# Kernel optimization log

Hardware: AMD Instinct MI355X
Metric: run time of the kernel (lower is better)

## Reference

```python
import jax, jax.numpy as jnp
import numpy as np

B, S, D = 8, 2048, 768

def setup_inputs() -> dict:
    key = jax.random.key(0)
    k1, k2, k3, k4 = jax.random.split(key, 4)
    scale = 1.0 / np.sqrt(D)
    x = jax.random.normal(k1, (B, S, D), dtype=jnp.float32)
    W = jax.random.normal(k2, (D, D), dtype=jnp.float32) * scale
    proj_w = jax.random.normal(k3, (D, D), dtype=jnp.float32) * scale
    proj_b = jax.random.normal(k4, (D,), dtype=jnp.float32) * scale
    return {"x": x, "W": W, "proj_w": proj_w, "proj_b": proj_b}


def reference(x, W, proj_w, proj_b):
    # Wx = Linear(x) with torch convention: x @ W.T  -> [B,S,D]
    Wx = jnp.einsum('bsd,ed->bse', x, W)
    # s = Wx @ x^T  -> [B,S,S]
    s = jnp.einsum('bse,bte->bst', Wx, x)
    # mask diagonal (self) with -inf
    eye = jnp.eye(S, dtype=bool)
    s = jnp.where(eye[None, :, :], -jnp.inf, s)
    a = jax.nn.softmax(s, axis=2)
    # c = a @ x -> [B,S,D]
    c = jnp.einsum('bst,btd->bsd', a, x)
    # proj + relu, residual; dropout with p=0 is identity
    c = jax.nn.relu(jnp.einsum('bsd,ed->bse', c, proj_w) + proj_b)
    return x + c
```

## Files before the change

### kernel.cpp

```cpp
#include <hip/hip_runtime.h>
#include <hip/hip_bf16.h>

typedef _Float16 fp16_t;
typedef __attribute__((ext_vector_type(8))) _Float16 fp16x8;
typedef __attribute__((ext_vector_type(4))) _Float16 fp16x4;
typedef __attribute__((ext_vector_type(4))) float fx4;

#define GLDS(g, l)                                                              \
  __builtin_amdgcn_global_load_lds(                                             \
      (const __attribute__((address_space(1))) void*)(g),                       \
      (__attribute__((address_space(3))) void*)(l), 16, 0, 0)

#define PBAR()                                                                  \
  do {                                                                          \
    __builtin_amdgcn_sched_barrier(0);                                          \
    __builtin_amdgcn_s_barrier();                                               \
    __builtin_amdgcn_sched_barrier(0);                                          \
  } while (0)

enum { EPI_F32 = 0, EPI_F16 = 1, EPI_FUSE = 2, EPI_SOFT = 3 };

__device__ __forceinline__ void xcd_decode(int& bx, int& by, int& bz) {
  const int nx = gridDim.x, ny = gridDim.y;
  const int lid = (int)(blockIdx.x + nx * (blockIdx.y + ny * blockIdx.z));
  const int j = lid & 7, k = lid >> 3;
  bx = k % nx;
  const int s = j + 8 * (k / nx);
  by = s % ny;
  bz = s / ny;
}

template <bool ASPLIT, int EPI>
__global__ __launch_bounds__(256) void gemm_bt(
    const fp16_t* __restrict__ A1, const fp16_t* __restrict__ A2,
    const fp16_t* __restrict__ B1, void* __restrict__ Cv, int K, int lda,
    int ldb, long long sA, long long sB, long long sC,
    const float* __restrict__ bias, const float* __restrict__ resid,
    float* __restrict__ m_out, float* __restrict__ l_out) {
  constexpr int ALO = ASPLIT ? 128 * 32 : 0;
  __shared__ __align__(16) fp16_t As[2][128 * 32 + ALO];
  __shared__ __align__(16) fp16_t Bs[2][128 * 32];
  __shared__ float smax[(EPI == EPI_SOFT) ? 256 : 1];
  __shared__ float ssum[(EPI == EPI_SOFT) ? 256 : 1];

  const int tid  = threadIdx.x;
  const int lane = tid & 63;
  const int w    = tid >> 6;
  const int wr   = w >> 1;
  const int wc   = w & 1;

  int bx, by, bz;
  xcd_decode(bx, by, bz);
  const int N = (int)gridDim.x * 128;
  const long long tile_m = (long long)by * 128;
  const long long tile_n = (long long)bx * 128;
  const long long z = bz;
  const long long aoff = z * sA + tile_m * (long long)lda;
  const long long boff = z * sB + tile_n * (long long)ldb;

  fx4 acc[4][4];
#pragma unroll
  for (int i = 0; i < 4; i++)
#pragma unroll
    for (int j = 0; j < 4; j++) acc[i][j] = (fx4){0.f, 0.f, 0.f, 0.f};

  const int r_l = lane >> 2;
  const int c_l = ((((lane & 3) + ((r_l >> 1) & 3)) & 3) << 3);
  const int frow = lane & 15;
  const int qoff = (((lane >> 4) - ((frow >> 1) & 3)) & 3) << 3;

  const size_t sa0 = (size_t)(w * 16 + r_l) * lda + c_l;
  const size_t sa1 = (size_t)(64 + w * 16 + r_l) * lda + c_l;
  const size_t sb0 = (size_t)(w * 16 + r_l) * ldb + c_l;
  const size_t sb1 = (size_t)(64 + w * 16 + r_l) * ldb + c_l;
  const int ld0 = (w * 16) * 32;
  const int ld1 = (64 + w * 16) * 32;

  auto stage = [&](int b, int kk) {
    const fp16_t* gah = A1 + aoff + kk;
    const fp16_t* gbh = B1 + boff + kk;
    GLDS(gah + sa0, &As[b][ld0]);
    GLDS(gah + sa1, &As[b][ld1]);
    GLDS(gbh + sb0, &Bs[b][ld0]);
    GLDS(gbh + sb1, &Bs[b][ld1]);
    if (ASPLIT) {
      const fp16_t* gal = A2 + aoff + kk;
      GLDS(gal + sa0, &As[b][ALO + ld0]);
      GLDS(gal + sa1, &As[b][ALO + ld1]);
    }
  };
  auto compute = [&](int b) {
    fp16x8 afh[4], bbh[4], afl[4];
#pragma unroll
    for (int mi = 0; mi < 4; mi++)
      afh[mi] = *(const fp16x8*)&As[b][(wr * 64 + mi * 16 + frow) * 32 + qoff];
#pragma unroll
    for (int ni = 0; ni < 4; ni++)
      bbh[ni] = *(const fp16x8*)&Bs[b][(wc * 64 + ni * 16 + frow) * 32 + qoff];
    if (ASPLIT) {
#pragma unroll
      for (int mi = 0; mi < 4; mi++)
        afl[mi] =
            *(const fp16x8*)&As[b][ALO + (wr * 64 + mi * 16 + frow) * 32 + qoff];
    }
#pragma unroll
    for (int mi = 0; mi < 4; mi++)
#pragma unroll
      for (int ni = 0; ni < 4; ni++) {
        fx4 a = acc[mi][ni];
        a = __builtin_amdgcn_mfma_f32_16x16x32_f16(afh[mi], bbh[ni], a, 0, 0, 0);
        if (ASPLIT)
          a = __builtin_amdgcn_mfma_f32_16x16x32_f16(afl[mi], bbh[ni], a, 0, 0, 0);
        acc[mi][ni] = a;
      }
  };

  stage(0, 0);
  for (int kt = 0; kt < K; kt += 64) {
    stage(1, kt + 32);
    if (ASPLIT) asm volatile("s_waitcnt vmcnt(6)" ::: "memory");
    else        asm volatile("s_waitcnt vmcnt(4)" ::: "memory");
    PBAR();
    compute(0);
    PBAR();
    if (kt + 64 < K) {
      stage(0, kt + 64);
      if (ASPLIT) asm volatile("s_waitcnt vmcnt(6)" ::: "memory");
      else        asm volatile("s_waitcnt vmcnt(4)" ::: "memory");
    } else {
      asm volatile("s_waitcnt vmcnt(0)" ::: "memory");
    }
    PBAR();
    compute(1);
    PBAR();
  }

  const int er = (lane >> 4) * 4;
  const int ec = lane & 15;
  const long long crow = tile_m + wr * 64;
  const long long ccol = tile_n + wc * 64;

  if constexpr (EPI == EPI_SOFT) {
#pragma unroll
    for (int mi = 0; mi < 4; mi++)
#pragma unroll
      for (int j = 0; j < 4; j++) {
        const long long r = crow + mi * 16 + er + j;
        float mx = -1e30f;
#pragma unroll
        for (int ni = 0; ni < 4; ni++) {
          const long long cc = ccol + ni * 16 + ec;
          float v = acc[mi][ni][j];
          if (r == cc) v = -1e30f;
          acc[mi][ni][j] = v;
          mx = fmaxf(mx, v);
        }
#pragma unroll
        for (int o = 1; o < 16; o <<= 1) mx = fmaxf(mx, __shfl_xor(mx, o, 64));
        if (ec == 0) smax[wc * 128 + wr * 64 + mi * 16 + er + j] = mx;
      }
    __syncthreads();
#pragma unroll
    for (int mi = 0; mi < 4; mi++)
#pragma unroll
      for (int j = 0; j < 4; j++) {
        const int rid = wr * 64 + mi * 16 + er + j;
        const float m = fmaxf(smax[rid], smax[128 + rid]);
        const long long r = crow + mi * 16 + er + j;
        float s = 0.f;
#pragma unroll
        for (int ni = 0; ni < 4; ni++) {
          const float e = __expf(acc[mi][ni][j] - m);
          s += e;
          ((fp16_t*)Cv)[z * sC + r * N + (ccol + ni * 16 + ec)] = (fp16_t)e;
        }
#pragma unroll
        for (int o = 1; o < 16; o <<= 1) s += __shfl_xor(s, o, 64);
        if (ec == 0) ssum[wc * 128 + rid] = s;
      }
    __syncthreads();
    if (tid < 128) {
      const long long si = (z * 16 + bx) * 2048 + tile_m + tid;
      m_out[si] = fmaxf(smax[tid], smax[128 + tid]);
      l_out[si] = ssum[tid] + ssum[128 + tid];
    }
  } else {
#pragma unroll
    for (int mi = 0; mi < 4; mi++)
#pragma unroll
      for (int j = 0; j < 4; j++) {
        const long long r = crow + mi * 16 + er + j;
#pragma unroll
        for (int ni = 0; ni < 4; ni++) {
          const long long cc = ccol + ni * 16 + ec;
          const long long idx = z * sC + r * N + cc;
          const float v = acc[mi][ni][j];
          if (EPI == EPI_F32) {
            ((float*)Cv)[idx] = v;
          } else if (EPI == EPI_F16) {
            ((fp16_t*)Cv)[idx] = (fp16_t)v;
          } else {
            float u = v + bias[cc];
            u = u > 0.f ? u : 0.f;
            ((float*)Cv)[idx] = resid[r * N + cc] + u;
          }
        }
      }
  }
}

__global__ __launch_bounds__(256) void gemm_pv(
    const fp16_t* __restrict__ P, const float* __restrict__ mstat,
    const float* __restrict__ lstat, const fp16_t* __restrict__ Bx,
    fp16_t* __restrict__ C) {
  __shared__ __align__(16) fp16_t As[2][128 * 32];
  __shared__ __align__(16) fp16_t Bs[2][128 * 32];
  __shared__ float sc[16][128];

  const int tid  = threadIdx.x;
  const int lane = tid & 63;
  const int w    = tid >> 6;
  const int wr   = w >> 1;
  const int wc   = w & 1;

  int bx, by, bz;
  xcd_decode(bx, by, bz);
  const long long tile_m = (long long)by * 128;
  const long long tile_n = (long long)bx * 128;
  const long long z = bz;

  if (tid < 128) {
    const long long base = z * 16 * 2048 + tile_m + tid;
    float mv[16];
    float m = -1e30f;
#pragma unroll
    for (int t = 0; t < 16; t++) {
      mv[t] = mstat[base + t * 2048];
      m = fmaxf(m, mv[t]);
    }
    float l = 0.f;
#pragma unroll
    for (int t = 0; t < 16; t++) l += lstat[base + t * 2048] * __expf(mv[t] - m);
    const float il = 1.0f / l;
#pragma unroll
    for (int t = 0; t < 16; t++) sc[t][tid] = __expf(mv[t] - m) * il;
  }
  __syncthreads();

  fx4 acc[4][4];
#pragma unroll
  for (int i = 0; i < 4; i++)
#pragma unroll
    for (int j = 0; j < 4; j++) acc[i][j] = (fx4){0.f, 0.f, 0.f, 0.f};

  const int r_l = lane >> 2;
  const int c_l = ((((lane & 3) + ((r_l >> 1) & 3)) & 3) << 3);
  const int frow = lane & 15;
  const int qoff = (((lane >> 4) - ((frow >> 1) & 3)) & 3) << 3;
  const size_t s0 = (size_t)(w * 16 + r_l) * 2048 + c_l;
  const size_t s1 = (size_t)(64 + w * 16 + r_l) * 2048 + c_l;
  const int ld0 = (w * 16) * 32;
  const int ld1 = (64 + w * 16) * 32;

  const fp16_t* A = P + z * (2048LL * 2048) + tile_m * 2048;
  const fp16_t* B = Bx + z * (768LL * 2048) + tile_n * 2048;

  auto stage = [&](int b, int kk) {
    GLDS(A + kk + s0, &As[b][ld0]);
    GLDS(A + kk + s1, &As[b][ld1]);
    GLDS(B + kk + s0, &Bs[b][ld0]);
    GLDS(B + kk + s1, &Bs[b][ld1]);
  };
  auto compute = [&](int b, const fp16_t* sh) {
    fp16x8 af[4], bb[4];
#pragma unroll
    for (int mi = 0; mi < 4; mi++) {
      af[mi] = *(const fp16x8*)&As[b][(wr * 64 + mi * 16 + frow) * 32 + qoff];
      af[mi] *= sh[mi];
    }
#pragma unroll
    for (int ni = 0; ni < 4; ni++)
      bb[ni] = *(const fp16x8*)&Bs[b][(wc * 64 + ni * 16 + frow) * 32 + qoff];
#pragma unroll
    for (int mi = 0; mi < 4; mi++)
#pragma unroll
      for (int ni = 0; ni < 4; ni++)
        acc[mi][ni] = __builtin_amdgcn_mfma_f32_16x16x32_f16(
            af[mi], bb[ni], acc[mi][ni], 0, 0, 0);
  };

  stage(0, 0);
  for (int kt = 0; kt < 2048; kt += 64) {
    fp16_t sh[4];
    {
      const int tt = kt >> 7;
#pragma unroll
      for (int mi = 0; mi < 4; mi++)
        sh[mi] = (fp16_t)sc[tt][wr * 64 + mi * 16 + frow];
    }
    stage(1, kt + 32);
    asm volatile("s_waitcnt vmcnt(4)" ::: "memory");
    PBAR();
    compute(0, sh);
    PBAR();
    if (kt + 64 < 2048) {
      stage(0, kt + 64);
      asm volatile("s_waitcnt vmcnt(4)" ::: "memory");
    } else {
      asm volatile("s_waitcnt vmcnt(0)" ::: "memory");
    }
    PBAR();
    compute(1, sh);
    PBAR();
  }

  const int er = (lane >> 4) * 4;
  const int ec = lane & 15;
  const long long crow = tile_m + wr * 64;
  const long long ccol = tile_n + wc * 64;
  fp16_t* Cz = C + z * (2048LL * 768);
#pragma unroll
  for (int mi = 0; mi < 4; mi++)
#pragma unroll
    for (int j = 0; j < 4; j++) {
      const long long rr = crow + mi * 16 + er + j;
#pragma unroll
      for (int ni = 0; ni < 4; ni++)
        Cz[rr * 768 + ccol + ni * 16 + ec] = (fp16_t)acc[mi][ni][j];
    }
}

__global__ __launch_bounds__(256) void prep_x(
    const float* __restrict__ x, fp16_t* __restrict__ xh,
    fp16_t* __restrict__ xl, fp16_t* __restrict__ xT) {
  __shared__ fp16_t t[32][33];
  const int b = blockIdx.z;
  const int d0 = blockIdx.x * 32;
  const int s0 = blockIdx.y * 32;
  const float* ib = x + (long long)b * 2048 * 768;
  const int tx = threadIdx.x & 31;
  const int ty = threadIdx.x >> 5;
#pragma unroll
  for (int i = 0; i < 4; i++) {
    const int srow = s0 + ty + i * 8;
    const long long idx = (long long)b * 2048 * 768 + (long long)srow * 768 + d0 + tx;
    const float v = ib[(long long)srow * 768 + d0 + tx];
    const fp16_t h = (fp16_t)v;
    xh[idx] = h;
    xl[idx] = (fp16_t)(v - (float)h);
    t[ty + i * 8][tx] = h;
  }
  __syncthreads();
#pragma unroll
  for (int i = 0; i < 4; i++)
    xT[(long long)b * 768 * 2048 + (long long)(d0 + ty + i * 8) * 2048 + s0 + tx] =
        t[tx][ty + i * 8];
}

__global__ __launch_bounds__(256) void cast2_f32_f16(
    const float* __restrict__ a, const float* __restrict__ b,
    fp16_t* __restrict__ oa, fp16_t* __restrict__ ob, int n4) {
  const int i = blockIdx.x * 256 + threadIdx.x;
  if (i >= n4) return;
  const float* in = blockIdx.y == 0 ? a : b;
  fp16_t* out = blockIdx.y == 0 ? oa : ob;
  const float4 v = ((const float4*)in)[i];
  ((fp16x4*)out)[i] =
      (fp16x4){(fp16_t)v.x, (fp16_t)v.y, (fp16_t)v.z, (fp16_t)v.w};
}

extern "C" void kernel_launch(void* const* d_in, const int* in_sizes, int n_in,
                              void* d_out, int out_size, void* d_ws,
                              size_t ws_size, hipStream_t stream) {
  const float* x  = (const float*)d_in[0];
  const float* W  = (const float*)d_in[1];
  const float* pw = (const float*)d_in[2];
  const float* pb = (const float*)d_in[3];

  const long long S = 2048, D = 768;
  const long long BS = 8 * S;

  char* p = (char*)d_ws;
  auto carve = [&](long long bytes) {
    char* q = p;
    p += (bytes + 255) & ~255LL;
    return q;
  };
  fp16_t* xh = (fp16_t*)carve(BS * D * 2);
  fp16_t* xl = (fp16_t*)carve(BS * D * 2);
  fp16_t* xT = (fp16_t*)carve(BS * D * 2);
  fp16_t* Wx = (fp16_t*)carve(BS * D * 2);
  fp16_t* Wh = (fp16_t*)carve(D * D * 2);
  fp16_t* ph = (fp16_t*)carve(D * D * 2);
  float*  mstat = (float*)carve(BS * 16 * 4);
  float*  lstat = (float*)carve(BS * 16 * 4);
  fp16_t* Ps = (fp16_t*)carve(8 * S * S * 2);
  fp16_t* cb = Wx;

  prep_x<<<dim3(24, 64, 8), 256, 0, stream>>>(x, xh, xl, xT);
  cast2_f32_f16<<<dim3((unsigned)(D * D / 4 / 256), 2), 256, 0, stream>>>(
      W, pw, Wh, ph, (int)(D * D / 4));

  gemm_bt<true, EPI_F16><<<dim3(6, 128, 1), 256, 0, stream>>>(
      xh, xl, Wh, Wx, 768, 768, 768, 0, 0, 0, nullptr, nullptr, nullptr,
      nullptr);

  gemm_bt<false, EPI_SOFT><<<dim3(16, 16, 8), 256, 0, stream>>>(
      Wx, nullptr, xh, Ps, 768, 768, 768, S * D, S * D, S * S, nullptr,
      nullptr, mstat, lstat);

  gemm_pv<<<dim3(6, 16, 8), 256, 0, stream>>>(Ps, mstat, lstat, xT, cb);

  gemm_bt<false, EPI_FUSE><<<dim3(6, 128, 1), 256, 0, stream>>>(
      cb, nullptr, ph, (float*)d_out, 768, 768, 768, 0, 0, 0, pb, x, nullptr,
      nullptr);
}
```

Measured before the change: 367.2 us.

## Simplify GEMM double-buffer loop to one barrier per k-step; overlap stats with prefetch

Both GEMM kernels drop the hand-tuned loop, which had a 64-wide k step, explicit vmcnt waits and four scheduling barriers per iteration. They now use a plain double buffer: each 32-wide k step issues the next stage's LDS loads, computes on the current buffer, then hits one __syncthreads. In the P·x kernel, the first tile load is now issued before the softmax-statistics reduction, so that global latency overlaps the scalar stat work. The aim is fewer barriers per k step, at the cost of losing fine-grained vmcnt control: __syncthreads waits for all outstanding loads every step.

```diff
diff --git a/kernel.cpp b/kernel.cpp
--- a/kernel.cpp
+++ b/kernel.cpp
@@ -10,13 +10,6 @@
   __builtin_amdgcn_global_load_lds(                                             \
       (const __attribute__((address_space(1))) void*)(g),                       \
       (__attribute__((address_space(3))) void*)(l), 16, 0, 0)
-
-#define PBAR()                                                                  \
-  do {                                                                          \
-    __builtin_amdgcn_sched_barrier(0);                                          \
-    __builtin_amdgcn_s_barrier();                                               \
-    __builtin_amdgcn_sched_barrier(0);                                          \
-  } while (0)
 
 enum { EPI_F32 = 0, EPI_F16 = 1, EPI_FUSE = 2, EPI_SOFT = 3 };
 
@@ -116,23 +109,13 @@
   };
 
   stage(0, 0);
-  for (int kt = 0; kt < K; kt += 64) {
-    stage(1, kt + 32);
-    if (ASPLIT) asm volatile("s_waitcnt vmcnt(6)" ::: "memory");
-    else        asm volatile("s_waitcnt vmcnt(4)" ::: "memory");
-    PBAR();
-    compute(0);
-    PBAR();
-    if (kt + 64 < K) {
-      stage(0, kt + 64);
-      if (ASPLIT) asm volatile("s_waitcnt vmcnt(6)" ::: "memory");
-      else        asm volatile("s_waitcnt vmcnt(4)" ::: "memory");
-    } else {
-      asm volatile("s_waitcnt vmcnt(0)" ::: "memory");
-    }
-    PBAR();
-    compute(1);
-    PBAR();
+  __syncthreads();
+  int cur = 0;
+  for (int kt = 0; kt < K; kt += 32) {
+    if (kt + 32 < K) stage(cur ^ 1, kt + 32);
+    compute(cur);
+    __syncthreads();
+    cur ^= 1;
   }
 
   const int er = (lane >> 4) * 4;
@@ -229,30 +212,6 @@
   const long long tile_n = (long long)bx * 128;
   const long long z = bz;
 
-  if (tid < 128) {
-    const long long base = z * 16 * 2048 + tile_m + tid;
-    float mv[16];
-    float m = -1e30f;
-#pragma unroll
-    for (int t = 0; t < 16; t++) {
-      mv[t] = mstat[base + t * 2048];
-      m = fmaxf(m, mv[t]);
-    }
-    float l = 0.f;
-#pragma unroll
-    for (int t = 0; t < 16; t++) l += lstat[base + t * 2048] * __expf(mv[t] - m);
-    const float il = 1.0f / l;
-#pragma unroll
-    for (int t = 0; t < 16; t++) sc[t][tid] = __expf(mv[t] - m) * il;
-  }
-  __syncthreads();
-
-  fx4 acc[4][4];
-#pragma unroll
-  for (int i = 0; i < 4; i++)
-#pragma unroll
-    for (int j = 0; j < 4; j++) acc[i][j] = (fx4){0.f, 0.f, 0.f, 0.f};
-
   const int r_l = lane >> 2;
   const int c_l = ((((lane & 3) + ((r_l >> 1) & 3)) & 3) << 3);
   const int frow = lane & 15;
@@ -271,6 +230,31 @@
     GLDS(B + kk + s0, &Bs[b][ld0]);
     GLDS(B + kk + s1, &Bs[b][ld1]);
   };
+
+  stage(0, 0);
+  if (tid < 128) {
+    const long long base = z * 16 * 2048 + tile_m + tid;
+    float mv[16];
+    float m = -1e30f;
+#pragma unroll
+    for (int t = 0; t < 16; t++) {
+      mv[t] = mstat[base + t * 2048];
+      m = fmaxf(m, mv[t]);
+    }
+    float l = 0.f;
+#pragma unroll
+    for (int t = 0; t < 16; t++) l += lstat[base + t * 2048] * __expf(mv[t] - m);
+    const float il = 1.0f / l;
+#pragma unroll
+    for (int t = 0; t < 16; t++) sc[t][tid] = __expf(mv[t] - m) * il;
+  }
+
+  fx4 acc[4][4];
+#pragma unroll
+  for (int i = 0; i < 4; i++)
+#pragma unroll
+    for (int j = 0; j < 4; j++) acc[i][j] = (fx4){0.f, 0.f, 0.f, 0.f};
+
   auto compute = [&](int b, const fp16_t* sh) {
     fp16x8 af[4], bb[4];
 #pragma unroll
@@ -289,8 +273,10 @@
             af[mi], bb[ni], acc[mi][ni], 0, 0, 0);
   };
 
-  stage(0, 0);
-  for (int kt = 0; kt < 2048; kt += 64) {
+  __syncthreads();
+  int cur = 0;
+  for (int kt = 0; kt < 2048; kt += 32) {
+    if (kt + 32 < 2048) stage(cur ^ 1, kt + 32);
     fp16_t sh[4];
     {
       const int tt = kt >> 7;
@@ -298,20 +284,9 @@
       for (int mi = 0; mi < 4; mi++)
         sh[mi] = (fp16_t)sc[tt][wr * 64 + mi * 16 + frow];
     }
-    stage(1, kt + 32);
-    asm volatile("s_waitcnt vmcnt(4)" ::: "memory");
-    PBAR();
-    compute(0, sh);
-    PBAR();
-    if (kt + 64 < 2048) {
-      stage(0, kt + 64);
-      asm volatile("s_waitcnt vmcnt(4)" ::: "memory");
-    } else {
-      asm volatile("s_waitcnt vmcnt(0)" ::: "memory");
-    }
-    PBAR();
-    compute(1, sh);
-    PBAR();
+    compute(cur, sh);
+    __syncthreads();
+    cur ^= 1;
   }
 
   const int er = (lane >> 4) * 4;
```

After: 380.8 us. 1.04x slower.
